# Optimization experiments

Hardware: AMD Instinct MI355X
Metric: run time of the kernel (lower is better)

Reference implementation:

```python
import jax, jax.numpy as jnp
import numpy as np

D_MODEL = 1024
NUM_HEADS = 16
D_K = D_MODEL // NUM_HEADS
TEMPERATURE = 1.0
LN_EPS = 1e-5


def setup_inputs() -> dict:
    key = jax.random.key(0)
    ks = jax.random.split(key, 12)
    B, S, D = 4, 1024, D_MODEL
    w = lambda k: jax.random.normal(k, (D, D), dtype=jnp.float32) * 0.02
    b = lambda k: jax.random.normal(k, (D,), dtype=jnp.float32) * 0.01
    return {
        "query": jax.random.normal(ks[0], (B, S, D), dtype=jnp.float32),
        "key": jax.random.normal(ks[1], (B, S, D), dtype=jnp.float32),
        "value": jax.random.normal(ks[2], (B, S, D), dtype=jnp.float32),
        "wq": w(ks[3]), "bq": b(ks[4]),
        "wk": w(ks[5]), "bk": b(ks[6]),
        "wv": w(ks[7]), "bv": b(ks[8]),
        "wo": w(ks[9]), "bo": b(ks[10]),
        "temporal_bias": jax.random.normal(ks[11], (1, 1, NUM_HEADS, 1, 1), dtype=jnp.float32) * 0.01,
        "adaptive_temp": jnp.ones((1,), dtype=jnp.float32),
        "ln_gamma": jnp.ones((D,), dtype=jnp.float32),
        "ln_beta": jnp.zeros((D,), dtype=jnp.float32),
    }


def reference(query, key, value, wq, bq, wk, bk, wv, bv, wo, bo,
              temporal_bias, adaptive_temp, ln_gamma, ln_beta):
    B, S, D = query.shape
    H, dk = NUM_HEADS, D_K
    # QKV projections -> (B, H, S, dk)
    Q = (query @ wq.T + bq).reshape(B, S, H, dk).transpose(0, 2, 1, 3)
    K = (key @ wk.T + bk).reshape(B, S, H, dk).transpose(0, 2, 1, 3)
    V = (value @ wv.T + bv).reshape(B, S, H, dk).transpose(0, 2, 1, 3)
    scores = jnp.einsum('bhqd,bhkd->bhqk', Q, K) / jnp.sqrt(jnp.float32(dk))
    scores = scores / (TEMPERATURE * adaptive_temp)
    # torch broadcasting bug reproduced: (B,H,S,S) + (1,1,H,1,1) -> (1,B,H,S,S)
    scores5 = scores[None, ...] + temporal_bias  # (1, B, H, S, S)
    attn = jax.nn.softmax(scores5, axis=-1)      # (1, B, H, S, S)
    ctx5 = jnp.einsum('xbhqk,bhkd->xbhqd', attn, V)  # (1, B, H, S, dk)
    # torch: transpose(1,2) -> (1, H, B, S, dk), then view(B, S, D)
    ctx = jnp.swapaxes(ctx5, 1, 2).reshape(B, S, D)
    out = ctx @ wo.T + bo
    y = out + query
    mu = jnp.mean(y, axis=-1, keepdims=True)
    var = jnp.mean(jnp.square(y - mu), axis=-1, keepdims=True)
    out_ln = (y - mu) / jnp.sqrt(var + LN_EPS) * ln_gamma + ln_beta
    return out_ln, attn
```

## Files before the change

kernel.cpp:

```cpp
#include <hip/hip_runtime.h>
#include <math.h>

#define BB 4
#define SS 1024
#define DD 1024
#define HH 16
#define DKK 64
#define NN (BB*SS)
#define LN_EPS 1e-5f
#define QB 64
#define JB 64

typedef __attribute__((ext_vector_type(8))) short bf16x8;
typedef __attribute__((ext_vector_type(4))) float f32x4;
typedef __attribute__((address_space(3))) unsigned int lds_u32;
typedef const __attribute__((address_space(1))) unsigned int glb_u32;

static __device__ __forceinline__ unsigned short f2bf(float x){
    unsigned int u = __float_as_uint(x);
    u += 0x7fff + ((u >> 16) & 1);
    return (unsigned short)(u >> 16);
}
static __device__ __forceinline__ int swzp(int q){
    return ((q & 7) << 4) ^ ((q & 8) << 2);
}

__global__ __launch_bounds__(256)
void k_cvt_in(const float* __restrict__ q, const float* __restrict__ k,
              const float* __restrict__ v, unsigned short* __restrict__ out){
    const int z = blockIdx.y;
    const float* src = (z == 0) ? q : (z == 1) ? k : v;
    const size_t i = ((size_t)blockIdx.x*256 + threadIdx.x)*8;
    float4 a = *reinterpret_cast<const float4*>(&src[i]);
    float4 b = *reinterpret_cast<const float4*>(&src[i+4]);
    int4 w;
    w.x = (int)((unsigned)f2bf(a.x) | ((unsigned)f2bf(a.y) << 16));
    w.y = (int)((unsigned)f2bf(a.z) | ((unsigned)f2bf(a.w) << 16));
    w.z = (int)((unsigned)f2bf(b.x) | ((unsigned)f2bf(b.y) << 16));
    w.w = (int)((unsigned)f2bf(b.z) | ((unsigned)f2bf(b.w) << 16));
    *reinterpret_cast<int4*>(&out[(size_t)z*NN*DD + i]) = w;
}

__global__ __launch_bounds__(256)
void k_cvt_w(const float* __restrict__ w0, const float* __restrict__ w1,
             const float* __restrict__ w2, const float* __restrict__ w3,
             unsigned short* __restrict__ out){
    const int z = blockIdx.y;
    const float* src = (z == 0) ? w0 : (z == 1) ? w1 : (z == 2) ? w2 : w3;
    const size_t i = ((size_t)blockIdx.x*256 + threadIdx.x)*8;
    float4 a = *reinterpret_cast<const float4*>(&src[i]);
    float4 b = *reinterpret_cast<const float4*>(&src[i+4]);
    int4 w;
    w.x = (int)((unsigned)f2bf(a.x) | ((unsigned)f2bf(a.y) << 16));
    w.y = (int)((unsigned)f2bf(a.z) | ((unsigned)f2bf(a.w) << 16));
    w.z = (int)((unsigned)f2bf(b.x) | ((unsigned)f2bf(b.y) << 16));
    w.w = (int)((unsigned)f2bf(b.z) | ((unsigned)f2bf(b.w) << 16));
    *reinterpret_cast<int4*>(&out[(size_t)z*DD*DD + i]) = w;
}

__global__ __launch_bounds__(256)
void k_gemmqkv(const unsigned short* __restrict__ Xb, const unsigned short* __restrict__ Wb,
               const float* __restrict__ b0, const float* __restrict__ b1,
               const float* __restrict__ b2, unsigned short* __restrict__ outb)
{
    __shared__ __align__(16) unsigned short Als[128*32];
    __shared__ __align__(16) unsigned short Bls[128*32];
    __shared__ __align__(16) unsigned short Cs[128*128];
    const int z = blockIdx.z;
    const unsigned short* X = Xb + (size_t)z*NN*DD;
    const unsigned short* W = Wb + (size_t)z*DD*DD;
    const float* bias = (z == 0) ? b0 : (z == 1) ? b1 : b2;
    unsigned short* out = outb + (size_t)z*NN*DD;

    const int row0 = blockIdx.x * 128;
    const int col0 = blockIdx.y * 128;
    const int t = threadIdx.x;
    const int w = t >> 6, l = t & 63;
    const int wr = w >> 1, wc = w & 1;

    f32x4 acc[4][4];
    #pragma unroll
    for (int m=0;m<4;++m)
        #pragma unroll
        for (int n=0;n<4;++n) acc[m][n] = (f32x4){0.f,0.f,0.f,0.f};

    const int srow  = l >> 2;
    const int skoff = (l & 3) * 8;

    for (int kt = 0; kt < DD; kt += 32) {
        #pragma unroll
        for (int i=0;i<2;++i) {
            const unsigned short* ga = X + (size_t)(row0 + w*32 + i*16 + srow)*DD + kt + skoff;
            const unsigned short* gb = W + (size_t)(col0 + w*32 + i*16 + srow)*DD + kt + skoff;
            __builtin_amdgcn_global_load_lds((glb_u32*)ga, (lds_u32*)&Als[(w*2+i)*512], 16, 0, 0);
            __builtin_amdgcn_global_load_lds((glb_u32*)gb, (lds_u32*)&Bls[(w*2+i)*512], 16, 0, 0);
        }
        __syncthreads();
        bf16x8 af[4], bfr[4];
        #pragma unroll
        for (int m=0;m<4;++m)
            af[m] = *reinterpret_cast<const bf16x8*>(&Als[(wr*64 + m*16 + (l&15))*32 + (l>>4)*8]);
        #pragma unroll
        for (int n=0;n<4;++n)
            bfr[n] = *reinterpret_cast<const bf16x8*>(&Bls[(wc*64 + n*16 + (l&15))*32 + (l>>4)*8]);
        __builtin_amdgcn_s_setprio(1);
        #pragma unroll
        for (int m=0;m<4;++m)
            #pragma unroll
            for (int n=0;n<4;++n)
                acc[m][n] = __builtin_amdgcn_mfma_f32_16x16x32_bf16(af[m], bfr[n], acc[m][n], 0, 0, 0);
        __builtin_amdgcn_s_setprio(0);
        __syncthreads();
    }

    if (z < 2) {
        #pragma unroll
        for (int m=0;m<4;++m){
            const int trb = wr*64 + m*16 + ((l>>4)<<2);
            #pragma unroll
            for (int n=0;n<4;++n){
                const int tc = wc*64 + n*16 + (l&15);
                const float bc = bias[col0 + tc];
                #pragma unroll
                for (int r=0;r<4;++r){
                    const int tr = trb + r;
                    *reinterpret_cast<unsigned short*>(
                        (char*)Cs + ((tr*256 + tc*2) ^ ((tr & 12) << 3))) = f2bf(acc[m][n][r] + bc);
                }
            }
        }
        __syncthreads();
        #pragma unroll
        for (int i=0;i<8;++i){
            const int slot = i*256 + t;
            const int r2 = slot >> 4, g = slot & 15;
            int4 v = *reinterpret_cast<const int4*>(
                (char*)Cs + ((r2*256 + g*16) ^ ((r2 & 12) << 3)));
            *reinterpret_cast<int4*>(&out[(size_t)(row0 + r2)*DD + col0 + g*8]) = v;
        }
    } else {
        #pragma unroll
        for (int m=0;m<4;++m){
            const int trb = wr*64 + m*16 + ((l>>4)<<2);
            #pragma unroll
            for (int n=0;n<4;++n){
                const int tc = wc*64 + n*16 + (l&15);
                const float bc = bias[col0 + tc];
                ushort4 pk;
                pk.x = f2bf(acc[m][n][0] + bc);
                pk.y = f2bf(acc[m][n][1] + bc);
                pk.z = f2bf(acc[m][n][2] + bc);
                pk.w = f2bf(acc[m][n][3] + bc);
                *reinterpret_cast<ushort4*>(
                    (char*)Cs + ((tc*256 + trb*2) ^ ((tc & 15) << 3))) = pk;
            }
        }
        __syncthreads();
        const int b = row0 >> 10;
        const int sbase = row0 & 1023;
        #pragma unroll
        for (int i=0;i<16;++i){
            const int cr = i*8 + (t>>5);
            const int ch = t & 31;
            ushort4 v = *reinterpret_cast<const ushort4*>(
                (char*)Cs + ((cr*256 + ch*8) ^ ((cr & 15) << 3)));
            const int gc = col0 + cr, h = gc >> 6, k = gc & 63;
            *reinterpret_cast<ushort4*>(
                &out[(((size_t)b*HH + h)*DKK + k)*SS + sbase + ch*4]) = v;
        }
    }
}

__global__ __launch_bounds__(256)
void k_attn(const unsigned short* __restrict__ Qb, const unsigned short* __restrict__ Kb,
            const unsigned short* __restrict__ Vtb, const float* __restrict__ at,
            float* __restrict__ attn, unsigned short* __restrict__ ctxb)
{
    __shared__ __align__(16) unsigned short Qs[QB*64];
    __shared__ __align__(16) unsigned short Ks[JB*64];
    __shared__ __align__(16) unsigned short Vs[DKK*JB];
    __shared__ __align__(16) unsigned short Ps[QB*JB];
    const int f  = blockIdx.x;
    const int wk2 = (f & 7)*128 + (f >> 3);
    const int bh = wk2 >> 4;
    const int q0 = (wk2 & 15) * QB;
    const int b = bh >> 4, h = bh & 15;
    const int t = threadIdx.x, w = t >> 6, l = t & 63;
    const float alpha = 0.125f / at[0];

    const unsigned short* Qg = Qb  + (size_t)b*SS*DD + (size_t)h*64;
    const unsigned short* Kg = Kb  + (size_t)b*SS*DD + (size_t)h*64;
    const unsigned short* Vg = Vtb + (size_t)bh*DKK*SS;

    #pragma unroll
    for (int p = 0; p < 2; ++p) {
        const int c = t + p*256;
        const int q = c >> 3, kc = (c & 7) * 8;
        int4 v = *reinterpret_cast<const int4*>(&Qg[(size_t)(q0 + q)*DD + kc]);
        *reinterpret_cast<int4*>((char*)Qs + ((q*128 + kc*2) ^ ((q & 7) << 4))) = v;
    }
    __syncthreads();
    bf16x8 qf[2];
    {
        const int q = w*16 + (l & 15);
        #pragma unroll
        for (int ks = 0; ks < 2; ++ks)
            qf[ks] = *reinterpret_cast<const bf16x8*>(
                (char*)Qs + ((q*128 + (l>>4)*16 + ks*64) ^ ((q & 7) << 4)));
    }

    float m[4], s[4];
    #pragma unroll
    for (int r = 0; r < 4; ++r) { m[r] = -1e30f; s[r] = 0.f; }

    for (int j0 = 0; j0 < SS; j0 += JB) {
        #pragma unroll
        for (int p = 0; p < 2; ++p) {
            const int c = t + p*256;
            const int j = c >> 3, kc = (c & 7) * 8;
            int4 v = *reinterpret_cast<const int4*>(&Kg[(size_t)(j0 + j)*DD + kc]);
            *reinterpret_cast<int4*>((char*)Ks + ((j*128 + kc*2) ^ ((j & 7) << 4))) = v;
        }
        __syncthreads();
        f32x4 acc[4];
        #pragma unroll
        for (int n = 0; n < 4; ++n) acc[n] = (f32x4){0.f,0.f,0.f,0.f};
        __builtin_amdgcn_s_setprio(1);
        #pragma unroll
        for (int ks = 0; ks < 2; ++ks) {
            #pragma unroll
            for (int n = 0; n < 4; ++n) {
                const int j = n*16 + (l & 15);
                bf16x8 kf = *reinterpret_cast<const bf16x8*>(
                    (char*)Ks + ((j*128 + (l>>4)*16 + ks*64) ^ ((j & 7) << 4)));
                acc[n] = __builtin_amdgcn_mfma_f32_16x16x32_bf16(qf[ks], kf, acc[n], 0, 0, 0);
            }
        }
        __builtin_amdgcn_s_setprio(0);
        #pragma unroll
        for (int r = 0; r < 4; ++r) {
            float tm = fmaxf(fmaxf(acc[0][r], acc[1][r]), fmaxf(acc[2][r], acc[3][r])) * alpha;
            #pragma unroll
            for (int off = 1; off < 16; off <<= 1)
                tm = fmaxf(tm, __shfl_xor(tm, off, 64));
            const float mn = fmaxf(m[r], tm);
            float ps = __expf(acc[0][r]*alpha - mn) + __expf(acc[1][r]*alpha - mn)
                     + __expf(acc[2][r]*alpha - mn) + __expf(acc[3][r]*alpha - mn);
            #pragma unroll
            for (int off = 1; off < 16; off <<= 1)
                ps += __shfl_xor(ps, off, 64);
            s[r] = s[r] * __expf(m[r] - mn) + ps;
            m[r] = mn;
        }
        __syncthreads();
    }

    float sinv[4];
    #pragma unroll
    for (int r = 0; r < 4; ++r) sinv[r] = 1.0f / s[r];

    f32x4 cacc[4];
    #pragma unroll
    for (int n = 0; n < 4; ++n) cacc[n] = (f32x4){0.f,0.f,0.f,0.f};

    for (int j0 = 0; j0 < SS; j0 += JB) {
        #pragma unroll
        for (int p = 0; p < 2; ++p) {
            const int c = t + p*256;
            const int j = c >> 3, kc = (c & 7) * 8;
            int4 v = *reinterpret_cast<const int4*>(&Kg[(size_t)(j0 + j)*DD + kc]);
            *reinterpret_cast<int4*>((char*)Ks + ((j*128 + kc*2) ^ ((j & 7) << 4))) = v;
            int4 vv = *reinterpret_cast<const int4*>(&Vg[(size_t)j*SS + j0 + kc]);
            *reinterpret_cast<int4*>((char*)Vs + ((j*128 + kc*2) ^ ((j & 7) << 4))) = vv;
        }
        __syncthreads();
        f32x4 acc[4];
        #pragma unroll
        for (int n = 0; n < 4; ++n) acc[n] = (f32x4){0.f,0.f,0.f,0.f};
        __builtin_amdgcn_s_setprio(1);
        #pragma unroll
        for (int ks = 0; ks < 2; ++ks) {
            #pragma unroll
            for (int n = 0; n < 4; ++n) {
                const int j = n*16 + (l & 15);
                bf16x8 kf = *reinterpret_cast<const bf16x8*>(
                    (char*)Ks + ((j*128 + (l>>4)*16 + ks*64) ^ ((j & 7) << 4)));
                acc[n] = __builtin_amdgcn_mfma_f32_16x16x32_bf16(qf[ks], kf, acc[n], 0, 0, 0);
            }
        }
        __builtin_amdgcn_s_setprio(0);
        #pragma unroll
        for (int n = 0; n < 4; ++n) {
            const int jl = n*16 + (l & 15);
            #pragma unroll
            for (int r = 0; r < 4; ++r) {
                const int q = w*16 + (l>>4)*4 + r;
                const float p = __expf(acc[n][r]*alpha - m[r]) * sinv[r];
                *reinterpret_cast<unsigned short*>(
                    (char*)Ps + ((q*128 + jl*2) ^ swzp(q))) = f2bf(p);
            }
        }
        __syncthreads();
        __builtin_amdgcn_s_setprio(1);
        #pragma unroll
        for (int ks = 0; ks < 2; ++ks) {
            const int qr = w*16 + (l & 15);
            bf16x8 pf = *reinterpret_cast<const bf16x8*>(
                (char*)Ps + ((qr*128 + (l>>4)*16 + ks*64) ^ swzp(qr)));
            #pragma unroll
            for (int n = 0; n < 4; ++n) {
                const int d = n*16 + (l & 15);
                bf16x8 vf = *reinterpret_cast<const bf16x8*>(
                    (char*)Vs + ((d*128 + (l>>4)*16 + ks*64) ^ ((d & 7) << 4)));
                cacc[n] = __builtin_amdgcn_mfma_f32_16x16x32_bf16(pf, vf, cacc[n], 0, 0, 0);
            }
        }
        __builtin_amdgcn_s_setprio(0);
        #pragma unroll
        for (int i = 0; i < 4; ++i) {
            const int sr = i*16 + (t >> 4);
            const int j4 = (t & 15) * 4;
            int2 u = *reinterpret_cast<const int2*>(
                (char*)Ps + ((sr*128 + j4*2) ^ swzp(sr)));
            f32x4 fv;
            fv.x = __uint_as_float(((unsigned)u.x) << 16);
            fv.y = __uint_as_float(((unsigned)u.x) & 0xffff0000u);
            fv.z = __uint_as_float(((unsigned)u.y) << 16);
            fv.w = __uint_as_float(((unsigned)u.y) & 0xffff0000u);
            __builtin_nontemporal_store(fv, reinterpret_cast<f32x4*>(
                &attn[((size_t)bh*SS + q0 + sr)*SS + j0 + j4]));
        }
        __syncthreads();
    }

    #pragma unroll
    for (int n = 0; n < 4; ++n) {
        const int d = n*16 + (l & 15);
        #pragma unroll
        for (int r = 0; r < 4; ++r) {
            const int q = q0 + w*16 + (l>>4)*4 + r;
            ctxb[(((size_t)h*BB + b)*SS + q)*DKK + d] = f2bf(cacc[n][r]);
        }
    }
}

__global__ __launch_bounds__(256)
void k_gemmo(const unsigned short* __restrict__ X, const unsigned short* __restrict__ W,
             const float* __restrict__ bias, const float* __restrict__ resid,
             float* __restrict__ outf)
{
    __shared__ __align__(16) unsigned short Als[128*32];
    __shared__ __align__(16) unsigned short Bls[128*32];
    const int row0 = blockIdx.x * 128;
    const int col0 = blockIdx.y * 128;
    const int t = threadIdx.x;
    const int w = t >> 6, l = t & 63;
    const int wr = w >> 1, wc = w & 1;

    f32x4 acc[4][4];
    #pragma unroll
    for (int m=0;m<4;++m)
        #pragma unroll
        for (int n=0;n<4;++n) acc[m][n] = (f32x4){0.f,0.f,0.f,0.f};

    const int srow  = l >> 2;
    const int skoff = (l & 3) * 8;

    for (int kt = 0; kt < DD; kt += 32) {
        #pragma unroll
        for (int i=0;i<2;++i) {
            const unsigned short* ga = X + (size_t)(row0 + w*32 + i*16 + srow)*DD + kt + skoff;
            const unsigned short* gb = W + (size_t)(col0 + w*32 + i*16 + srow)*DD + kt + skoff;
            __builtin_amdgcn_global_load_lds((glb_u32*)ga, (lds_u32*)&Als[(w*2+i)*512], 16, 0, 0);
            __builtin_amdgcn_global_load_lds((glb_u32*)gb, (lds_u32*)&Bls[(w*2+i)*512], 16, 0, 0);
        }
        __syncthreads();
        bf16x8 af[4], bfr[4];
        #pragma unroll
        for (int m=0;m<4;++m)
            af[m] = *reinterpret_cast<const bf16x8*>(&Als[(wr*64 + m*16 + (l&15))*32 + (l>>4)*8]);
        #pragma unroll
        for (int n=0;n<4;++n)
            bfr[n] = *reinterpret_cast<const bf16x8*>(&Bls[(wc*64 + n*16 + (l&15))*32 + (l>>4)*8]);
        __builtin_amdgcn_s_setprio(1);
        #pragma unroll
        for (int m=0;m<4;++m)
            #pragma unroll
            for (int n=0;n<4;++n)
                acc[m][n] = __builtin_amdgcn_mfma_f32_16x16x32_bf16(af[m], bfr[n], acc[m][n], 0, 0, 0);
        __builtin_amdgcn_s_setprio(0);
        __syncthreads();
    }

    #pragma unroll
    for (int m=0;m<4;++m){
        const int grow_base = row0 + wr*64 + m*16 + ((l>>4)<<2);
        #pragma unroll
        for (int n=0;n<4;++n){
            const int col = col0 + wc*64 + n*16 + (l&15);
            const float bc = bias[col];
            #pragma unroll
            for (int r=0;r<4;++r){
                const int row = grow_base + r;
                outf[(size_t)row*DD + col] = acc[m][n][r] + bc + resid[(size_t)row*DD + col];
            }
        }
    }
}

__global__ __launch_bounds__(256)
void k_ln(const float* __restrict__ y, const float* __restrict__ g,
          const float* __restrict__ be, float* __restrict__ out)
{
    const int row = blockIdx.x;
    const int t = threadIdx.x;
    float4 v = *reinterpret_cast<const float4*>(&y[(size_t)row*DD + t*4]);
    float s  = v.x + v.y + v.z + v.w;
    float ss = v.x*v.x + v.y*v.y + v.z*v.z + v.w*v.w;
    #pragma unroll
    for (int off = 32; off > 0; off >>= 1) {
        s  += __shfl_xor(s,  off, 64);
        ss += __shfl_xor(ss, off, 64);
    }
    __shared__ float red[8];
    const int lane = t & 63, wid = t >> 6;
    if (lane == 0) { red[wid] = s; red[4+wid] = ss; }
    __syncthreads();
    const float S1 = red[0]+red[1]+red[2]+red[3];
    const float S2 = red[4]+red[5]+red[6]+red[7];
    const float mu  = S1 * (1.0f/DD);
    const float var = fmaxf(S2 * (1.0f/DD) - mu*mu, 0.0f);
    const float rstd = rsqrtf(var + LN_EPS);
    float4 gv = *reinterpret_cast<const float4*>(&g[t*4]);
    float4 bv = *reinterpret_cast<const float4*>(&be[t*4]);
    float4 o;
    o.x = (v.x - mu)*rstd*gv.x + bv.x;
    o.y = (v.y - mu)*rstd*gv.y + bv.y;
    o.z = (v.z - mu)*rstd*gv.z + bv.z;
    o.w = (v.w - mu)*rstd*gv.w + bv.w;
    *reinterpret_cast<float4*>(&out[(size_t)row*DD + t*4]) = o;
}

extern "C" void kernel_launch(void* const* d_in, const int* in_sizes, int n_in,
                              void* d_out, int out_size, void* d_ws, size_t ws_size,
                              hipStream_t stream) {
    const float* query = (const float*)d_in[0];
    const float* key   = (const float*)d_in[1];
    const float* value = (const float*)d_in[2];
    const float* wq = (const float*)d_in[3];
    const float* bq = (const float*)d_in[4];
    const float* wk = (const float*)d_in[5];
    const float* bk = (const float*)d_in[6];
    const float* wv = (const float*)d_in[7];
    const float* bv = (const float*)d_in[8];
    const float* wo = (const float*)d_in[9];
    const float* bo = (const float*)d_in[10];
    const float* at = (const float*)d_in[12];
    const float* g  = (const float*)d_in[13];
    const float* be = (const float*)d_in[14];

    float* out_ln = (float*)d_out;
    float* attn   = (float*)d_out + (size_t)NN*DD;

    char* wsb = (char*)d_ws;
    unsigned short* xq   = (unsigned short*)(wsb);
    unsigned short* Qb   = (unsigned short*)(wsb + ((size_t)24<<20));
    unsigned short* Kb   = (unsigned short*)(wsb + ((size_t)32<<20));
    unsigned short* Vtb  = (unsigned short*)(wsb + ((size_t)40<<20));
    unsigned short* ctxb = (unsigned short*)(wsb + ((size_t)48<<20));
    unsigned short* wqb  = (unsigned short*)(wsb + ((size_t)56<<20));
    float*          y    = (float*)(wsb);

    k_cvt_in<<<dim3(2048, 3), 256, 0, stream>>>(query, key, value, xq);
    k_cvt_w<<<dim3(512, 4), 256, 0, stream>>>(wq, wk, wv, wo, wqb);

    k_gemmqkv<<<dim3(32, 8, 3), 256, 0, stream>>>(xq, wqb, bq, bk, bv, Qb);

    k_attn<<<dim3(1024), 256, 0, stream>>>(Qb, Kb, Vtb, at, attn, ctxb);

    k_gemmo<<<dim3(32, 8), 256, 0, stream>>>(ctxb, wqb + (size_t)3*DD*DD, bo, query, y);

    k_ln<<<NN, 256, 0, stream>>>(y, g, be, out_ln);
}
```

Before: 190.8 us.

## Enlarge attention query tile, prefetch K/V tiles in registers, merge conversion kernels

Result: faster. 186.1 us (-2.5%).

```diff
diff --git a/kernel.cpp b/kernel.cpp
--- a/kernel.cpp
+++ b/kernel.cpp
@@ -8,7 +8,7 @@
 #define DKK 64
 #define NN (BB*SS)
 #define LN_EPS 1e-5f
-#define QB 64
+#define QB 128
 #define JB 64
 
 typedef __attribute__((ext_vector_type(8))) short bf16x8;
@@ -26,11 +26,24 @@
 }
 
 __global__ __launch_bounds__(256)
-void k_cvt_in(const float* __restrict__ q, const float* __restrict__ k,
-              const float* __restrict__ v, unsigned short* __restrict__ out){
-    const int z = blockIdx.y;
-    const float* src = (z == 0) ? q : (z == 1) ? k : v;
-    const size_t i = ((size_t)blockIdx.x*256 + threadIdx.x)*8;
+void k_cvt_all(const float* __restrict__ q, const float* __restrict__ k,
+               const float* __restrict__ v, const float* __restrict__ w0,
+               const float* __restrict__ w1, const float* __restrict__ w2,
+               const float* __restrict__ w3, unsigned short* __restrict__ xout,
+               unsigned short* __restrict__ wout){
+    const int bidx = blockIdx.x;
+    const float* src; unsigned short* dst; size_t i;
+    if (bidx < 6144) {
+        const int z = bidx >> 11, bi = bidx & 2047;
+        src = (z == 0) ? q : (z == 1) ? k : v;
+        dst = xout + (size_t)z*NN*DD;
+        i = ((size_t)bi*256 + threadIdx.x)*8;
+    } else {
+        const int z = (bidx - 6144) >> 9, bi = (bidx - 6144) & 511;
+        src = (z == 0) ? w0 : (z == 1) ? w1 : (z == 2) ? w2 : w3;
+        dst = wout + (size_t)z*DD*DD;
+        i = ((size_t)bi*256 + threadIdx.x)*8;
+    }
     float4 a = *reinterpret_cast<const float4*>(&src[i]);
     float4 b = *reinterpret_cast<const float4*>(&src[i+4]);
     int4 w;
@@ -38,24 +51,7 @@
     w.y = (int)((unsigned)f2bf(a.z) | ((unsigned)f2bf(a.w) << 16));
     w.z = (int)((unsigned)f2bf(b.x) | ((unsigned)f2bf(b.y) << 16));
     w.w = (int)((unsigned)f2bf(b.z) | ((unsigned)f2bf(b.w) << 16));
-    *reinterpret_cast<int4*>(&out[(size_t)z*NN*DD + i]) = w;
-}
-
-__global__ __launch_bounds__(256)
-void k_cvt_w(const float* __restrict__ w0, const float* __restrict__ w1,
-             const float* __restrict__ w2, const float* __restrict__ w3,
-             unsigned short* __restrict__ out){
-    const int z = blockIdx.y;
-    const float* src = (z == 0) ? w0 : (z == 1) ? w1 : (z == 2) ? w2 : w3;
-    const size_t i = ((size_t)blockIdx.x*256 + threadIdx.x)*8;
-    float4 a = *reinterpret_cast<const float4*>(&src[i]);
-    float4 b = *reinterpret_cast<const float4*>(&src[i+4]);
-    int4 w;
-    w.x = (int)((unsigned)f2bf(a.x) | ((unsigned)f2bf(a.y) << 16));
-    w.y = (int)((unsigned)f2bf(a.z) | ((unsigned)f2bf(a.w) << 16));
-    w.z = (int)((unsigned)f2bf(b.x) | ((unsigned)f2bf(b.y) << 16));
-    w.w = (int)((unsigned)f2bf(b.z) | ((unsigned)f2bf(b.w) << 16));
-    *reinterpret_cast<int4*>(&out[(size_t)z*DD*DD + i]) = w;
+    *reinterpret_cast<int4*>(&dst[i]) = w;
 }
 
 __global__ __launch_bounds__(256)
@@ -171,7 +167,7 @@
     }
 }
 
-__global__ __launch_bounds__(256)
+__global__ __launch_bounds__(512)
 void k_attn(const unsigned short* __restrict__ Qb, const unsigned short* __restrict__ Kb,
             const unsigned short* __restrict__ Vtb, const float* __restrict__ at,
             float* __restrict__ attn, unsigned short* __restrict__ ctxb)
@@ -180,10 +176,10 @@
     __shared__ __align__(16) unsigned short Ks[JB*64];
     __shared__ __align__(16) unsigned short Vs[DKK*JB];
     __shared__ __align__(16) unsigned short Ps[QB*JB];
-    const int f  = blockIdx.x;
-    const int wk2 = (f & 7)*128 + (f >> 3);
-    const int bh = wk2 >> 4;
-    const int q0 = (wk2 & 15) * QB;
+    const int f   = blockIdx.x;
+    const int wk2 = (f & 7)*64 + (f >> 3);
+    const int bh  = wk2 >> 3;
+    const int q0  = (wk2 & 7) * QB;
     const int b = bh >> 4, h = bh & 15;
     const int t = threadIdx.x, w = t >> 6, l = t & 63;
     const float alpha = 0.125f / at[0];
@@ -192,12 +188,19 @@
     const unsigned short* Kg = Kb  + (size_t)b*SS*DD + (size_t)h*64;
     const unsigned short* Vg = Vtb + (size_t)bh*DKK*SS;
 
+    const int sj  = t >> 3;
+    const int skc = (t & 7) * 8;
+
     #pragma unroll
     for (int p = 0; p < 2; ++p) {
-        const int c = t + p*256;
+        const int c = t + p*512;
         const int q = c >> 3, kc = (c & 7) * 8;
         int4 v = *reinterpret_cast<const int4*>(&Qg[(size_t)(q0 + q)*DD + kc]);
         *reinterpret_cast<int4*>((char*)Qs + ((q*128 + kc*2) ^ ((q & 7) << 4))) = v;
+    }
+    {
+        int4 kv = *reinterpret_cast<const int4*>(&Kg[(size_t)sj*DD + skc]);
+        *reinterpret_cast<int4*>((char*)Ks + ((sj*128 + skc*2) ^ ((sj & 7) << 4))) = kv;
     }
     __syncthreads();
     bf16x8 qf[2];
@@ -214,14 +217,9 @@
     for (int r = 0; r < 4; ++r) { m[r] = -1e30f; s[r] = 0.f; }
 
     for (int j0 = 0; j0 < SS; j0 += JB) {
-        #pragma unroll
-        for (int p = 0; p < 2; ++p) {
-            const int c = t + p*256;
-            const int j = c >> 3, kc = (c & 7) * 8;
-            int4 v = *reinterpret_cast<const int4*>(&Kg[(size_t)(j0 + j)*DD + kc]);
-            *reinterpret_cast<int4*>((char*)Ks + ((j*128 + kc*2) ^ ((j & 7) << 4))) = v;
-        }
-        __syncthreads();
+        int4 knext;
+        if (j0 + JB < SS)
+            knext = *reinterpret_cast<const int4*>(&Kg[(size_t)(j0 + JB + sj)*DD + skc]);
         f32x4 acc[4];
         #pragma unroll
         for (int n = 0; n < 4; ++n) acc[n] = (f32x4){0.f,0.f,0.f,0.f};
@@ -253,6 +251,10 @@
             m[r] = mn;
         }
         __syncthreads();
+        if (j0 + JB < SS) {
+            *reinterpret_cast<int4*>((char*)Ks + ((sj*128 + skc*2) ^ ((sj & 7) << 4))) = knext;
+        }
+        __syncthreads();
     }
 
     float sinv[4];
@@ -263,17 +265,20 @@
     #pragma unroll
     for (int n = 0; n < 4; ++n) cacc[n] = (f32x4){0.f,0.f,0.f,0.f};
 
+    {
+        int4 kv = *reinterpret_cast<const int4*>(&Kg[(size_t)sj*DD + skc]);
+        int4 vv = *reinterpret_cast<const int4*>(&Vg[(size_t)sj*SS + skc]);
+        *reinterpret_cast<int4*>((char*)Ks + ((sj*128 + skc*2) ^ ((sj & 7) << 4))) = kv;
+        *reinterpret_cast<int4*>((char*)Vs + ((sj*128 + skc*2) ^ ((sj & 7) << 4))) = vv;
+    }
+    __syncthreads();
+
     for (int j0 = 0; j0 < SS; j0 += JB) {
-        #pragma unroll
-        for (int p = 0; p < 2; ++p) {
-            const int c = t + p*256;
-            const int j = c >> 3, kc = (c & 7) * 8;
-            int4 v = *reinterpret_cast<const int4*>(&Kg[(size_t)(j0 + j)*DD + kc]);
-            *reinterpret_cast<int4*>((char*)Ks + ((j*128 + kc*2) ^ ((j & 7) << 4))) = v;
-            int4 vv = *reinterpret_cast<const int4*>(&Vg[(size_t)j*SS + j0 + kc]);
-            *reinterpret_cast<int4*>((char*)Vs + ((j*128 + kc*2) ^ ((j & 7) << 4))) = vv;
-        }
-        __syncthreads();
+        int4 knext, vnext;
+        if (j0 + JB < SS) {
+            knext = *reinterpret_cast<const int4*>(&Kg[(size_t)(j0 + JB + sj)*DD + skc]);
+            vnext = *reinterpret_cast<const int4*>(&Vg[(size_t)sj*SS + j0 + JB + skc]);
+        }
         f32x4 acc[4];
         #pragma unroll
         for (int n = 0; n < 4; ++n) acc[n] = (f32x4){0.f,0.f,0.f,0.f};
@@ -318,7 +323,7 @@
         __builtin_amdgcn_s_setprio(0);
         #pragma unroll
         for (int i = 0; i < 4; ++i) {
-            const int sr = i*16 + (t >> 4);
+            const int sr = i*32 + (t >> 4);
             const int j4 = (t & 15) * 4;
             int2 u = *reinterpret_cast<const int2*>(
                 (char*)Ps + ((sr*128 + j4*2) ^ swzp(sr)));
@@ -329,6 +334,11 @@
             fv.w = __uint_as_float(((unsigned)u.y) & 0xffff0000u);
             __builtin_nontemporal_store(fv, reinterpret_cast<f32x4*>(
                 &attn[((size_t)bh*SS + q0 + sr)*SS + j0 + j4]));
+        }
+        __syncthreads();
+        if (j0 + JB < SS) {
+            *reinterpret_cast<int4*>((char*)Ks + ((sj*128 + skc*2) ^ ((sj & 7) << 4))) = knext;
+            *reinterpret_cast<int4*>((char*)Vs + ((sj*128 + skc*2) ^ ((sj & 7) << 4))) = vnext;
         }
         __syncthreads();
     }
@@ -471,12 +481,11 @@
     unsigned short* wqb  = (unsigned short*)(wsb + ((size_t)56<<20));
     float*          y    = (float*)(wsb);
 
-    k_cvt_in<<<dim3(2048, 3), 256, 0, stream>>>(query, key, value, xq);
-    k_cvt_w<<<dim3(512, 4), 256, 0, stream>>>(wq, wk, wv, wo, wqb);
+    k_cvt_all<<<8192, 256, 0, stream>>>(query, key, value, wq, wk, wv, wo, xq, wqb);
 
     k_gemmqkv<<<dim3(32, 8, 3), 256, 0, stream>>>(xq, wqb, bq, bk, bv, Qb);
 
-    k_attn<<<dim3(1024), 256, 0, stream>>>(Qb, Kb, Vtb, at, attn, ctxb);
+    k_attn<<<dim3(512), 512, 0, stream>>>(Qb, Kb, Vtb, at, attn, ctxb);
 
     k_gemmo<<<dim3(32, 8), 256, 0, stream>>>(ctxb, wqb + (size_t)3*DD*DD, bo, query, y);
 
```
